# Kernel optimization log

Measured on AMD Instinct MI355X. Metric: run time of the kernel, lower is better.

Reference implementation:

```python
import jax, jax.numpy as jnp
import numpy as np
import math


def _attn(q, k, v):
    # q,k,v: [B, S, d] (d == 1 here). bmm -> scale -> softmax -> bmm.
    scale = 1.0 / math.sqrt(q.shape[2])
    e = jnp.einsum('bsd,btd->bst', q, k) * scale  # [B, S, S]
    w = jax.nn.softmax(e, axis=2)
    return jnp.einsum('bst,btd->bsd', w, v)


def setup_inputs() -> dict:
    key = jax.random.key(0)
    ks = jax.random.split(key, 12)
    B, D = 32, 768
    CLF_OUT = 7
    inp = {}
    names = ['sentence', 'target_spkr_snts', 'other_spkr_snts', 'scene_desc', 'scene_sent']
    for i, name in enumerate(names):
        inp[name] = jax.random.normal(ks[i], (B, D), dtype=jnp.float32)
    inp['W_shared'] = jax.random.normal(ks[5], (768, 512), dtype=jnp.float32) * 0.02
    inp['b_shared'] = jnp.zeros((512,), dtype=jnp.float32)
    inp['W1'] = jax.random.normal(ks[6], (3840, 256), dtype=jnp.float32) * 0.02
    inp['b1'] = jnp.zeros((256,), dtype=jnp.float32)
    inp['W2'] = jax.random.normal(ks[7], (256, CLF_OUT), dtype=jnp.float32) * 0.02
    inp['b2'] = jnp.zeros((CLF_OUT,), dtype=jnp.float32)
    return inp


def reference(sentence, target_spkr_snts, other_spkr_snts, scene_desc, scene_sent,
              W_shared, b_shared, W1, b1, W2, b2):
    B = sentence.shape[0]
    s = sentence[..., None]             # [B, 768, 1]
    sd = scene_desc[..., None]
    ts = target_spkr_snts[..., None]
    oth = other_spkr_snts[..., None]
    ss = scene_sent[..., None]

    speaker_context = _attn(oth, ts, ts)   # [B, 768, 1]
    scene_context = _attn(ss, ss, sd)      # [B, 768, 1]

    sentence_shared = sentence @ W_shared + b_shared                     # [B, 512]
    scene_context_shared = scene_context.reshape(B, -1) @ W_shared + b_shared
    speaker_context_shared = speaker_context.reshape(B, -1) @ W_shared + b_shared

    fused = jnp.concatenate([s, scene_context, speaker_context], axis=1)  # [B, 2304, 1]
    z = _attn(fused, fused, fused)                                        # [B, 2304, 1]

    final = jnp.concatenate([z.reshape(B, -1), sentence_shared,
                             scene_context_shared, speaker_context_shared], axis=1)  # [B, 3840]
    h = jax.nn.relu(final @ W1 + b1)   # dropout is identity in eval mode
    return jax.nn.sigmoid(h @ W2 + b2)  # [B, 7]
```

## Files before the change

kernel.cpp:

```cpp
#include <hip/hip_runtime.h>
#include <math.h>

#define NPOW 88
#define NCO  85


__device__ __forceinline__ void proj_256(
    const float* __restrict__ xsrc,
    const float* __restrict__ Ws,
    const float* __restrict__ bs,
    float* __restrict__ dst,
    float* xb,
    float* redf,
    int tid)
{
    for (int i = tid; i < 768; i += 256) xb[i] = xsrc[i];
    __syncthreads();

    const int g = tid >> 7;
    const int q = tid & 127;
    const float4* __restrict__ Wv = (const float4*)Ws;
    float ax = 0.f, ay = 0.f, az = 0.f, aw = 0.f;
    #pragma unroll 8
    for (int k = g; k < 768; k += 2) {
        const float xv = xb[k];
        const float4 w = Wv[k * 128 + q];
        ax += xv * w.x; ay += xv * w.y; az += xv * w.z; aw += xv * w.w;
    }
    redf[g * 512 + q * 4 + 0] = ax;
    redf[g * 512 + q * 4 + 1] = ay;
    redf[g * 512 + q * 4 + 2] = az;
    redf[g * 512 + q * 4 + 3] = aw;
    __syncthreads();

    dst[tid]       = bs[tid]       + redf[tid]       + redf[512 + tid];
    dst[tid + 256] = bs[tid + 256] + redf[tid + 256] + redf[512 + tid + 256];
}

__device__ __forceinline__ double red32(double x) {
    x += __shfl_xor(x, 1, 64);
    x += __shfl_xor(x, 2, 64);
    x += __shfl_xor(x, 4, 64);
    x += __shfl_xor(x, 8, 64);
    x += __shfl_xor(x, 16, 64);
    return x;
}

__global__ __launch_bounds__(256) void k1_small_kernel(
    const float* __restrict__ sentence,
    const float* __restrict__ target,
    const float* __restrict__ other,
    const float* __restrict__ scene_desc,
    const float* __restrict__ scene_sent,
    const float* __restrict__ Ws,
    const float* __restrict__ bs,
    float* __restrict__ ctx,
    float* __restrict__ final_)
{
    const int b = blockIdx.x;
    const int y = blockIdx.y;
    const int tid = threadIdx.x;
    __shared__ float kb[768];
    __shared__ float vbuf[768];
    __shared__ double redbuf[2][2048];
    __shared__ double part[NPOW][2];
    __shared__ double coefA[NCO];
    __shared__ double coefB[NCO];
    __shared__ float redf[1024];

    if (y == 2) {
        proj_256(sentence + b * 768, Ws, bs, final_ + b * 3840 + 2304, kb, redf, tid);
        return;
    }

    const bool scene = (y == 0);
    const float* kp = scene ? (scene_sent + b * 768) : (target + b * 768);
    const float* vp = scene ? (scene_desc + b * 768) : (target + b * 768);
    for (int i = tid; i < 768; i += 256) { kb[i] = kp[i]; vbuf[i] = vp[i]; }
    __syncthreads();

    const double k0 = (double)kb[tid], k1 = (double)kb[tid + 256], k2 = (double)kb[tid + 512];
    const double v0 = (double)vbuf[tid], v1 = (double)vbuf[tid + 256], v2 = (double)vbuf[tid + 512];
    double p0 = 1.0, p1 = 1.0, p2 = 1.0;

    if (scene) {
        for (int c = 0; c < 22; ++c) {
            double* buf = redbuf[c & 1];
            #pragma unroll
            for (int m = 0; m < 4; ++m) {
                buf[(m * 2 + 0) * 256 + tid] = (p0 + p1) + p2;
                buf[(m * 2 + 1) * 256 + tid] = fma(p0, v0, fma(p1, v1, p2 * v2));
                p0 *= k0; p1 *= k1; p2 *= k2;
            }
            __syncthreads();
            const int n = tid >> 6;
            const int s = (tid >> 5) & 1;
            const int l = tid & 31;
            const double* src = buf + (n * 2 + s) * 256 + l;
            double acc = ((src[0] + src[32]) + (src[64] + src[96]))
                       + ((src[128] + src[160]) + (src[192] + src[224]));
            acc = red32(acc);
            if (l == 0) part[c * 4 + n][s] = acc;
        }
    } else {
        for (int c = 0; c < 11; ++c) {
            double* buf = redbuf[c & 1];
            #pragma unroll
            for (int m = 0; m < 8; ++m) {
                buf[m * 256 + tid] = (p0 + p1) + p2;
                p0 *= k0; p1 *= k1; p2 *= k2;
            }
            __syncthreads();
            const int n = tid >> 5;
            const int l = tid & 31;
            const double* src = buf + n * 256 + l;
            double acc = ((src[0] + src[32]) + (src[64] + src[96]))
                       + ((src[128] + src[160]) + (src[192] + src[224]));
            acc = red32(acc);
            if (l == 0) part[c * 8 + n][0] = acc;
        }
    }
    __syncthreads();

    if (tid < NCO) {
        double fact = 1.0;
        for (int i = 2; i <= tid; ++i) fact *= (double)i;
        const double inv = 1.0 / fact;
        coefA[tid] = part[tid][0] * inv;
        coefB[tid] = scene ? (part[tid][1] * inv) : (part[tid + 1][0] * inv);
    }
    __syncthreads();

    double q[3], num[3], den[3];
    #pragma unroll
    for (int j = 0; j < 3; ++j) {
        const int r = tid + 256 * j;
        q[j] = scene ? (double)kb[r] : (double)other[b * 768 + r];
        den[j] = coefA[NCO - 1];
        num[j] = coefB[NCO - 1];
    }
    for (int n = NCO - 2; n >= 0; --n) {
        const double a = coefA[n], cc = coefB[n];
        #pragma unroll
        for (int j = 0; j < 3; ++j) {
            den[j] = fma(den[j], q[j], a);
            num[j] = fma(num[j], q[j], cc);
        }
    }
    #pragma unroll
    for (int j = 0; j < 3; ++j)
        ctx[b * 1536 + (scene ? 0 : 768) + tid + 256 * j] = (float)(num[j] / den[j]);
}

__global__ __launch_bounds__(256) void k2_fused_kernel(
    const float* __restrict__ sentence,
    const float* __restrict__ ctx,
    const float* __restrict__ Ws,
    const float* __restrict__ bs,
    float* __restrict__ final_)
{
    const int b = blockIdx.x;
    const int y = blockIdx.y;
    const int tid = threadIdx.x;
    __shared__ float fb[2304];
    __shared__ double redbuf[2][2048];
    __shared__ double part[NPOW];
    __shared__ double coefA[NCO];
    __shared__ double coefB[NCO];
    __shared__ float redf[1024];

    if (y > 0) {
        proj_256(ctx + b * 1536 + (y - 1) * 768, Ws, bs,
                 final_ + b * 3840 + 2304 + y * 512, fb, redf, tid);
        return;
    }

    for (int i = tid; i < 2304; i += 256)
        fb[i] = (i < 768) ? sentence[b * 768 + i] : ctx[b * 1536 + (i - 768)];
    __syncthreads();

    double kv[9], pw[9];
    #pragma unroll
    for (int j = 0; j < 9; ++j) { kv[j] = (double)fb[tid + 256 * j]; pw[j] = 1.0; }

    for (int c = 0; c < 11; ++c) {
        double* buf = redbuf[c & 1];
        #pragma unroll
        for (int m = 0; m < 8; ++m) {
            buf[m * 256 + tid] = (((pw[0] + pw[1]) + (pw[2] + pw[3]))
                                + ((pw[4] + pw[5]) + (pw[6] + pw[7]))) + pw[8];
            #pragma unroll
            for (int j = 0; j < 9; ++j) pw[j] *= kv[j];
        }
        __syncthreads();
        const int n = tid >> 5;
        const int l = tid & 31;
        const double* src = buf + n * 256 + l;
        double acc = ((src[0] + src[32]) + (src[64] + src[96]))
                   + ((src[128] + src[160]) + (src[192] + src[224]));
        acc = red32(acc);
        if (l == 0) part[c * 8 + n] = acc;
    }
    __syncthreads();

    if (tid < NCO) {
        double fact = 1.0;
        for (int i = 2; i <= tid; ++i) fact *= (double)i;
        const double inv = 1.0 / fact;
        coefA[tid] = part[tid] * inv;
        coefB[tid] = part[tid + 1] * inv;
    }
    __syncthreads();

    double num[9], den[9];
    #pragma unroll
    for (int j = 0; j < 9; ++j) { den[j] = coefA[NCO - 1]; num[j] = coefB[NCO - 1]; }
    for (int n = NCO - 2; n >= 0; --n) {
        const double a = coefA[n], cc = coefB[n];
        #pragma unroll
        for (int j = 0; j < 9; ++j) {
            den[j] = fma(den[j], kv[j], a);
            num[j] = fma(num[j], kv[j], cc);
        }
    }
    #pragma unroll
    for (int j = 0; j < 9; ++j)
        final_[b * 3840 + tid + 256 * j] = (float)(num[j] / den[j]);
}

__global__ __launch_bounds__(1024) void mlp_part_kernel(
    const float* __restrict__ final_,
    const float* __restrict__ W1,
    float* __restrict__ hpart)
{
    const int b = blockIdx.x;
    const int c = blockIdx.y;
    const int tid = threadIdx.x;
    const int base = c * 480;

    __shared__ float fb[480];
    __shared__ float red[16][256];
    if (tid < 480) fb[tid] = final_[b * 3840 + base + tid];
    __syncthreads();

    const int g = tid >> 6;
    const int q = tid & 63;
    const float4* __restrict__ Wv = (const float4*)W1;
    float ax = 0.f, ay = 0.f, az = 0.f, aw = 0.f;
    const int l0 = g * 30;
    #pragma unroll 5
    for (int kk = 0; kk < 30; ++kk) {
        const float xv = fb[l0 + kk];
        const float4 w = Wv[(base + l0 + kk) * 64 + q];
        ax += xv * w.x; ay += xv * w.y; az += xv * w.z; aw += xv * w.w;
    }
    red[g][q * 4 + 0] = ax;
    red[g][q * 4 + 1] = ay;
    red[g][q * 4 + 2] = az;
    red[g][q * 4 + 3] = aw;
    __syncthreads();

    if (tid < 256) {
        float s = 0.f;
        #pragma unroll
        for (int g2 = 0; g2 < 16; ++g2) s += red[g2][tid];
        hpart[(b * 8 + c) * 256 + tid] = s;
    }
}

__global__ __launch_bounds__(512) void mlp_tail_kernel(
    const float* __restrict__ hpart,
    const float* __restrict__ b1,
    const float* __restrict__ W2,
    const float* __restrict__ b2,
    float* __restrict__ out)
{
    const int b = blockIdx.x;
    const int tid = threadIdx.x;

    __shared__ float hb[256];
    if (tid < 256) {
        float s = b1[tid];
        #pragma unroll
        for (int c = 0; c < 8; ++c) s += hpart[(b * 8 + c) * 256 + tid];
        hb[tid] = fmaxf(s, 0.f);
    }
    __syncthreads();

    const int w = tid >> 6;
    const int lane = tid & 63;
    if (w < 7) {
        float a = 0.f;
        #pragma unroll
        for (int c = lane; c < 256; c += 64)
            a += hb[c] * W2[c * 7 + w];
        #pragma unroll
        for (int off = 32; off > 0; off >>= 1)
            a += __shfl_down(a, off, 64);
        if (lane == 0)
            out[b * 7 + w] = 1.f / (1.f + __expf(-(a + b2[w])));
    }
}

extern "C" void kernel_launch(void* const* d_in, const int* in_sizes, int n_in,
                              void* d_out, int out_size, void* d_ws, size_t ws_size,
                              hipStream_t stream) {
    const float* sentence   = (const float*)d_in[0];
    const float* target     = (const float*)d_in[1];
    const float* other      = (const float*)d_in[2];
    const float* scene_desc = (const float*)d_in[3];
    const float* scene_sent = (const float*)d_in[4];
    const float* Ws         = (const float*)d_in[5];
    const float* bs         = (const float*)d_in[6];
    const float* W1         = (const float*)d_in[7];
    const float* b1         = (const float*)d_in[8];
    const float* W2         = (const float*)d_in[9];
    const float* b2         = (const float*)d_in[10];
    float* out = (float*)d_out;

    float* ctx    = (float*)d_ws;
    float* final_ = ctx + 32 * 1536;
    float* hpart  = final_ + 32 * 3840;

    k1_small_kernel<<<dim3(32, 3), 256, 0, stream>>>(sentence, target, other,
                                                     scene_desc, scene_sent,
                                                     Ws, bs, ctx, final_);
    k2_fused_kernel<<<dim3(32, 3), 256, 0, stream>>>(sentence, ctx, Ws, bs, final_);
    mlp_part_kernel<<<dim3(32, 8), 1024, 0, stream>>>(final_, W1, hpart);
    mlp_tail_kernel<<<32, 512, 0, stream>>>(hpart, b1, W2, b2, out);
}
```

Measured before the change: 52.51 us.

## Use fp32 power sums with scaled keys and split Horner evaluation across blocks

After: 50.66 us. 1.04x faster.

```diff
diff --git a/kernel.cpp b/kernel.cpp
--- a/kernel.cpp
+++ b/kernel.cpp
@@ -1,9 +1,18 @@
 #include <hip/hip_runtime.h>
 #include <math.h>
 
+
 #define NPOW 88
 #define NCO  85
 
+__device__ __forceinline__ float red32f(float x) {
+    x += __shfl_xor(x, 1, 64);
+    x += __shfl_xor(x, 2, 64);
+    x += __shfl_xor(x, 4, 64);
+    x += __shfl_xor(x, 8, 64);
+    x += __shfl_xor(x, 16, 64);
+    return x;
+}
 
 __device__ __forceinline__ void proj_256(
     const float* __restrict__ xsrc,
@@ -35,15 +44,6 @@
 
     dst[tid]       = bs[tid]       + redf[tid]       + redf[512 + tid];
     dst[tid + 256] = bs[tid + 256] + redf[tid + 256] + redf[512 + tid + 256];
-}
-
-__device__ __forceinline__ double red32(double x) {
-    x += __shfl_xor(x, 1, 64);
-    x += __shfl_xor(x, 2, 64);
-    x += __shfl_xor(x, 4, 64);
-    x += __shfl_xor(x, 8, 64);
-    x += __shfl_xor(x, 16, 64);
-    return x;
 }
 
 __global__ __launch_bounds__(256) void k1_small_kernel(
@@ -62,62 +62,60 @@
     const int tid = threadIdx.x;
     __shared__ float kb[768];
     __shared__ float vbuf[768];
-    __shared__ double redbuf[2][2048];
-    __shared__ double part[NPOW][2];
+    __shared__ float redbuf[2][2048];
+    __shared__ float partS[NPOW];
+    __shared__ float partT[NPOW];
     __shared__ double coefA[NCO];
     __shared__ double coefB[NCO];
     __shared__ float redf[1024];
 
-    if (y == 2) {
+    if (y == 6) {
         proj_256(sentence + b * 768, Ws, bs, final_ + b * 3840 + 2304, kb, redf, tid);
         return;
     }
 
-    const bool scene = (y == 0);
+    const bool scene = (y < 3);
     const float* kp = scene ? (scene_sent + b * 768) : (target + b * 768);
     const float* vp = scene ? (scene_desc + b * 768) : (target + b * 768);
     for (int i = tid; i < 768; i += 256) { kb[i] = kp[i]; vbuf[i] = vp[i]; }
     __syncthreads();
 
-    const double k0 = (double)kb[tid], k1 = (double)kb[tid + 256], k2 = (double)kb[tid + 512];
-    const double v0 = (double)vbuf[tid], v1 = (double)vbuf[tid + 256], v2 = (double)vbuf[tid + 512];
-    double p0 = 1.0, p1 = 1.0, p2 = 1.0;
+    const float g0 = kb[tid] * 0.25f, g1 = kb[tid + 256] * 0.25f, g2 = kb[tid + 512] * 0.25f;
+    float p0 = 1.f, p1 = 1.f, p2 = 1.f;
 
     if (scene) {
+        const float v0 = vbuf[tid], v1 = vbuf[tid + 256], v2 = vbuf[tid + 512];
         for (int c = 0; c < 22; ++c) {
-            double* buf = redbuf[c & 1];
+            float* buf = redbuf[c & 1];
             #pragma unroll
             for (int m = 0; m < 4; ++m) {
                 buf[(m * 2 + 0) * 256 + tid] = (p0 + p1) + p2;
-                buf[(m * 2 + 1) * 256 + tid] = fma(p0, v0, fma(p1, v1, p2 * v2));
-                p0 *= k0; p1 *= k1; p2 *= k2;
+                buf[(m * 2 + 1) * 256 + tid] = fmaf(p0, v0, fmaf(p1, v1, p2 * v2));
+                p0 *= g0; p1 *= g1; p2 *= g2;
             }
             __syncthreads();
-            const int n = tid >> 6;
-            const int s = (tid >> 5) & 1;
-            const int l = tid & 31;
-            const double* src = buf + (n * 2 + s) * 256 + l;
-            double acc = ((src[0] + src[32]) + (src[64] + src[96]))
-                       + ((src[128] + src[160]) + (src[192] + src[224]));
-            acc = red32(acc);
-            if (l == 0) part[c * 4 + n][s] = acc;
+            const int n = tid >> 6, s = (tid >> 5) & 1, l = tid & 31;
+            const float* src = buf + (n * 2 + s) * 256 + l;
+            float acc = ((src[0] + src[32]) + (src[64] + src[96]))
+                      + ((src[128] + src[160]) + (src[192] + src[224]));
+            acc = red32f(acc);
+            if (l == 0) { if (s == 0) partS[c * 4 + n] = acc; else partT[c * 4 + n] = acc; }
         }
     } else {
         for (int c = 0; c < 11; ++c) {
-            double* buf = redbuf[c & 1];
+            float* buf = redbuf[c & 1];
             #pragma unroll
             for (int m = 0; m < 8; ++m) {
                 buf[m * 256 + tid] = (p0 + p1) + p2;
-                p0 *= k0; p1 *= k1; p2 *= k2;
+                p0 *= g0; p1 *= g1; p2 *= g2;
             }
             __syncthreads();
-            const int n = tid >> 5;
-            const int l = tid & 31;
-            const double* src = buf + n * 256 + l;
-            double acc = ((src[0] + src[32]) + (src[64] + src[96]))
-                       + ((src[128] + src[160]) + (src[192] + src[224]));
-            acc = red32(acc);
-            if (l == 0) part[c * 8 + n][0] = acc;
+            const int n = tid >> 5, l = tid & 31;
+            const float* src = buf + n * 256 + l;
+            float acc = ((src[0] + src[32]) + (src[64] + src[96]))
+                      + ((src[128] + src[160]) + (src[192] + src[224]));
+            acc = red32f(acc);
+            if (l == 0) partS[c * 8 + n] = acc;
         }
     }
     __syncthreads();
@@ -126,30 +124,21 @@
         double fact = 1.0;
         for (int i = 2; i <= tid; ++i) fact *= (double)i;
         const double inv = 1.0 / fact;
-        coefA[tid] = part[tid][0] * inv;
-        coefB[tid] = scene ? (part[tid][1] * inv) : (part[tid + 1][0] * inv);
-    }
-    __syncthreads();
-
-    double q[3], num[3], den[3];
-    #pragma unroll
-    for (int j = 0; j < 3; ++j) {
-        const int r = tid + 256 * j;
-        q[j] = scene ? (double)kb[r] : (double)other[b * 768 + r];
-        den[j] = coefA[NCO - 1];
-        num[j] = coefB[NCO - 1];
-    }
+        coefA[tid] = (double)partS[tid] * inv;
+        coefB[tid] = scene ? ((double)partT[tid] * inv) : ((double)partS[tid + 1] * inv);
+    }
+    __syncthreads();
+
+    const int slice = scene ? y : (y - 3);
+    const int r = slice * 256 + tid;
+    const double x = 4.0 * (double)(scene ? kb[r] : other[b * 768 + r]);
+    double den = coefA[NCO - 1], num = coefB[NCO - 1];
     for (int n = NCO - 2; n >= 0; --n) {
-        const double a = coefA[n], cc = coefB[n];
-        #pragma unroll
-        for (int j = 0; j < 3; ++j) {
-            den[j] = fma(den[j], q[j], a);
-            num[j] = fma(num[j], q[j], cc);
-        }
-    }
-    #pragma unroll
-    for (int j = 0; j < 3; ++j)
-        ctx[b * 1536 + (scene ? 0 : 768) + tid + 256 * j] = (float)(num[j] / den[j]);
+        den = fma(den, x, coefA[n]);
+        num = fma(num, x, coefB[n]);
+    }
+    const double ratio = scene ? (num / den) : (4.0 * num / den);
+    ctx[b * 1536 + (scene ? 0 : 768) + r] = (float)ratio;
 }
 
 __global__ __launch_bounds__(256) void k2_fused_kernel(
@@ -163,15 +152,16 @@
     const int y = blockIdx.y;
     const int tid = threadIdx.x;
     __shared__ float fb[2304];
-    __shared__ double redbuf[2][2048];
-    __shared__ double part[NPOW];
+    __shared__ float redbuf[2][2048];
+    __shared__ float partS[NPOW];
     __shared__ double coefA[NCO];
     __shared__ double coefB[NCO];
     __shared__ float redf[1024];
 
-    if (y > 0) {
-        proj_256(ctx + b * 1536 + (y - 1) * 768, Ws, bs,
-                 final_ + b * 3840 + 2304 + y * 512, fb, redf, tid);
+    if (y >= 9) {
+        const int p = y - 8;
+        proj_256(ctx + b * 1536 + (p - 1) * 768, Ws, bs,
+                 final_ + b * 3840 + 2304 + p * 512, fb, redf, tid);
         return;
     }
 
@@ -179,27 +169,26 @@
         fb[i] = (i < 768) ? sentence[b * 768 + i] : ctx[b * 1536 + (i - 768)];
     __syncthreads();
 
-    double kv[9], pw[9];
+    float g[9], pw[9];
     #pragma unroll
-    for (int j = 0; j < 9; ++j) { kv[j] = (double)fb[tid + 256 * j]; pw[j] = 1.0; }
+    for (int j = 0; j < 9; ++j) { g[j] = fb[tid + 256 * j] * 0.25f; pw[j] = 1.f; }
 
     for (int c = 0; c < 11; ++c) {
-        double* buf = redbuf[c & 1];
+        float* buf = redbuf[c & 1];
         #pragma unroll
         for (int m = 0; m < 8; ++m) {
             buf[m * 256 + tid] = (((pw[0] + pw[1]) + (pw[2] + pw[3]))
                                 + ((pw[4] + pw[5]) + (pw[6] + pw[7]))) + pw[8];
             #pragma unroll
-            for (int j = 0; j < 9; ++j) pw[j] *= kv[j];
+            for (int j = 0; j < 9; ++j) pw[j] *= g[j];
         }
         __syncthreads();
-        const int n = tid >> 5;
-        const int l = tid & 31;
-        const double* src = buf + n * 256 + l;
-        double acc = ((src[0] + src[32]) + (src[64] + src[96]))
-                   + ((src[128] + src[160]) + (src[192] + src[224]));
-        acc = red32(acc);
-        if (l == 0) part[c * 8 + n] = acc;
+        const int n = tid >> 5, l = tid & 31;
+        const float* src = buf + n * 256 + l;
+        float acc = ((src[0] + src[32]) + (src[64] + src[96]))
+                  + ((src[128] + src[160]) + (src[192] + src[224]));
+        acc = red32f(acc);
+        if (l == 0) partS[c * 8 + n] = acc;
     }
     __syncthreads();
 
@@ -207,25 +196,19 @@
         double fact = 1.0;
         for (int i = 2; i <= tid; ++i) fact *= (double)i;
         const double inv = 1.0 / fact;
-        coefA[tid] = part[tid] * inv;
-        coefB[tid] = part[tid + 1] * inv;
-    }
-    __syncthreads();
-
-    double num[9], den[9];
-    #pragma unroll
-    for (int j = 0; j < 9; ++j) { den[j] = coefA[NCO - 1]; num[j] = coefB[NCO - 1]; }
+        coefA[tid] = (double)partS[tid] * inv;
+        coefB[tid] = (double)partS[tid + 1] * inv;
+    }
+    __syncthreads();
+
+    const int r = y * 256 + tid;
+    const double x = 4.0 * (double)fb[r];
+    double den = coefA[NCO - 1], num = coefB[NCO - 1];
     for (int n = NCO - 2; n >= 0; --n) {
-        const double a = coefA[n], cc = coefB[n];
-        #pragma unroll
-        for (int j = 0; j < 9; ++j) {
-            den[j] = fma(den[j], kv[j], a);
-            num[j] = fma(num[j], kv[j], cc);
-        }
-    }
-    #pragma unroll
-    for (int j = 0; j < 9; ++j)
-        final_[b * 3840 + tid + 256 * j] = (float)(num[j] / den[j]);
+        den = fma(den, x, coefA[n]);
+        num = fma(num, x, coefB[n]);
+    }
+    final_[b * 3840 + r] = (float)(4.0 * num / den);
 }
 
 __global__ __launch_bounds__(1024) void mlp_part_kernel(
@@ -322,10 +305,10 @@
     float* final_ = ctx + 32 * 1536;
     float* hpart  = final_ + 32 * 3840;
 
-    k1_small_kernel<<<dim3(32, 3), 256, 0, stream>>>(sentence, target, other,
+    k1_small_kernel<<<dim3(32, 7), 256, 0, stream>>>(sentence, target, other,
                                                      scene_desc, scene_sent,
                                                      Ws, bs, ctx, final_);
-    k2_fused_kernel<<<dim3(32, 3), 256, 0, stream>>>(sentence, ctx, Ws, bs, final_);
+    k2_fused_kernel<<<dim3(32, 11), 256, 0, stream>>>(sentence, ctx, Ws, bs, final_);
     mlp_part_kernel<<<dim3(32, 8), 1024, 0, stream>>>(final_, W1, hpart);
     mlp_tail_kernel<<<32, 512, 0, stream>>>(hpart, b1, W2, b2, out);
 }
```
